# Kernel tuning notes

Hardware: AMD Instinct MI355X
Metric: run time of the kernel (lower is better)

## Reference

```python
import jax, jax.numpy as jnp
import numpy as np

# ---- static configuration (mirrors repo globals) ----
D_MODEL = 1024   # d_model
B = 128          # batch size
T = 256          # structure sequence length (tgt)
T_C = 128        # max constraints per scene (tgt_c rows)
N_PER = 64       # real (non-padded) constraints per scene
S = 128          # number of source objects per scene (src_e rows)
N_TYPES = 4      # len(constraint_types)
N_DIR = 4        # len(direction_types)
C_TOKEN = 2      # structure_vocab_map['c']
N_C = N_PER * B  # total constraints across the batch (static!)


def setup_inputs() -> dict:
    key = jax.random.key(0)
    ks = jax.random.split(key, 12)
    decoded_output = jax.random.normal(ks[0], (T, B, D_MODEL), jnp.float32)
    # tgt: the first N_PER timesteps of every batch element are constraint tokens 'c'.
    tgt = jnp.where(jnp.arange(T)[:, None] < N_PER, C_TOKEN, 0) * jnp.ones((1, B), jnp.int32)
    tgt = tgt.astype(jnp.int32)
    # tgt_c padding: rows >= N_PER are padding -> exactly N_PER*B = N_C real constraints,
    # laid out row-major (timestep-major, batch-fastest) when flattened.
    tgt_c_padding_mask = jnp.broadcast_to(jnp.arange(T_C)[:, None] >= N_PER, (T_C, B))
    types_col = jax.random.randint(ks[1], (T_C, B), 0, N_TYPES)
    q_col = jax.random.randint(ks[2], (T_C, B), 0, S)
    r_col = jax.random.randint(ks[3], (T_C, B), 0, S)
    tgt_c = jnp.stack([types_col, q_col, r_col], axis=-1).astype(jnp.int32)  # [T_C,B,3]
    src_e = jax.random.normal(ks[4], (S, B, D_MODEL), jnp.float32)
    src_padding_mask = jax.random.uniform(ks[5], (B, S)) < 0.1
    scale = 0.02
    params = {
        'type_emb': jax.random.normal(ks[6], (N_TYPES, D_MODEL), jnp.float32),
        'W_ctype': jax.random.normal(ks[7], (N_TYPES, D_MODEL), jnp.float32) * scale,
        'b_ctype': jnp.zeros((N_TYPES,), jnp.float32),
        'W_obj': jax.random.normal(ks[8], (D_MODEL, 3 * D_MODEL), jnp.float32) * scale,
        'b_obj': jnp.zeros((D_MODEL,), jnp.float32),
        'W_dir': jax.random.normal(ks[9], (N_DIR, 4 * D_MODEL), jnp.float32) * scale,
        'b_dir': jnp.zeros((N_DIR,), jnp.float32),
    }
    return dict(decoded_output=decoded_output, tgt=tgt, tgt_c=tgt_c,
                tgt_c_padding_mask=tgt_c_padding_mask, src_e=src_e,
                src_padding_mask=src_padding_mask, **params)


def reference(decoded_output, tgt, tgt_c, tgt_c_padding_mask, src_e, src_padding_mask,
              type_emb, W_ctype, b_ctype, W_obj, b_obj, W_dir, b_dir):
    d = decoded_output.shape[-1]
    # --- static-count boolean selections (setup guarantees exactly N_C True entries) ---
    idx_struct = jnp.nonzero((tgt == C_TOKEN).reshape(-1), size=N_C)[0]
    heads = decoded_output.reshape(-1, d)[idx_struct]                # [N_C, d]
    idx_c = jnp.nonzero((~tgt_c_padding_mask).reshape(-1), size=N_C)[0]

    # constraint type logits
    type_selections = heads @ W_ctype.T + b_ctype                    # [N_C, N_TYPES]

    # constraint type embeddings
    types = type_emb[tgt_c[:, :, 0].reshape(-1)[idx_c]]              # [N_C, d]

    # q_e: gather query-object embeddings (torch.gather along dim 0)
    q_idx = jnp.broadcast_to(tgt_c[:, :, 1:2], (T_C, B, d))
    q_e = jnp.take_along_axis(src_e, q_idx, axis=0).reshape(-1, d)[idx_c]  # [N_C, d]

    obj_in = jnp.concatenate([heads, types, q_e], axis=1)            # [N_C, 3d]
    pointer = obj_in @ W_obj.T + b_obj                               # [N_C, d]

    batch_ref = jnp.broadcast_to(jnp.arange(B), (T_C, B)).reshape(-1)[idx_c]  # [N_C]
    # Setup layout guarantee: flattened constraint order is (t, b) row-major with b
    # fastest, N_PER constraints per batch -> pointer reshapes to [N_PER, B, d] and the
    # original per-item tensordot loop collapses into one batched einsum.
    ptr = pointer.reshape(N_PER, B, d)
    logits = jnp.einsum('tbd,sbd->tbs', ptr, src_e).reshape(N_C, S)  # [N_C, S]
    object_selections = jnp.where(src_padding_mask[batch_ref], -jnp.inf, logits)

    # r_e: gather reference-object embeddings
    r_idx = jnp.broadcast_to(tgt_c[:, :, 2:3], (T_C, B, d))
    r_e = jnp.take_along_axis(src_e, r_idx, axis=0).reshape(-1, d)[idx_c]    # [N_C, d]

    dir_in = jnp.concatenate([obj_in, r_e], axis=1)                  # [N_C, 4d]
    direction_selections = dir_in @ W_dir.T + b_dir                  # [N_C, N_DIR]
    return (type_selections, object_selections, direction_selections)
```

## Files before the change

### kernel.cpp

```cpp
#include <hip/hip_runtime.h>
#include <hip/hip_bf16.h>
#include <math.h>

#define D_MODEL 1024
#define B_SZ    128
#define S_SZ    128
#define N_C     8192
#define K_OBJ   3072
#define K_DIR   4096

#define TS_OFF  0
#define OS_OFF  (N_C * 4)
#define DS_OFF  (OS_OFF + N_C * S_SZ)

#define NEG_BIG (-1.0e30f)

typedef __attribute__((ext_vector_type(8))) int   i32x8;
typedef __attribute__((ext_vector_type(4))) float f32x4;

#define WS_PTR8   0ull
#define WS_DEC8   8388608ull
#define WS_SRCE8  16777216ull
#define WS_WOBJ8  33554432ull
#define WS_TEMB8  36700160ull

#define SCALE_ONE 0x7F7F7F7F

__device__ __forceinline__ uint2 f32x8_to_fp8(float4 a, float4 b) {
    unsigned lo = 0, hi = 0;
    lo = __builtin_amdgcn_cvt_pk_fp8_f32(a.x, a.y, lo, false);
    lo = __builtin_amdgcn_cvt_pk_fp8_f32(a.z, a.w, lo, true);
    hi = __builtin_amdgcn_cvt_pk_fp8_f32(b.x, b.y, hi, false);
    hi = __builtin_amdgcn_cvt_pk_fp8_f32(b.z, b.w, hi, true);
    return make_uint2(lo, hi);
}
__device__ __forceinline__ unsigned char f32_to_fp8(float x) {
    return (unsigned char)(__builtin_amdgcn_cvt_pk_fp8_f32(x, x, 0, false) & 0xFF);
}

typedef __attribute__((address_space(3))) unsigned int lds_u32;
typedef __attribute__((address_space(1))) const unsigned int glb_u32;
__device__ __forceinline__ void dma16(const void* g, void* l) {
    __builtin_amdgcn_global_load_lds((glb_u32*)g, (lds_u32*)l, 16, 0, 0);
}

__global__ __launch_bounds__(256) void cvt_fp8_all(
    const float* __restrict__ decoded, const float* __restrict__ src_e,
    const float* __restrict__ W_obj,   const float* __restrict__ type_emb,
    unsigned char* __restrict__ dec8,  unsigned char* __restrict__ srce8,
    unsigned char* __restrict__ wobj8, unsigned char* __restrict__ temb8)
{
    const int blk = blockIdx.x;
    const float* src; unsigned char* dst; size_t u;
    if (blk < 4096)        { src = decoded;  dst = dec8;  u = (size_t)blk * 256 + threadIdx.x; }
    else if (blk < 12288)  { src = src_e;    dst = srce8; u = (size_t)(blk - 4096) * 256 + threadIdx.x; }
    else if (blk < 13824)  { src = W_obj;    dst = wobj8; u = (size_t)(blk - 12288) * 256 + threadIdx.x; }
    else                   { src = type_emb; dst = temb8; u = (size_t)(blk - 13824) * 256 + threadIdx.x; }
    const float4* s = (const float4*)src + u * 2;
    float4 a = s[0], b = s[1];
    *(uint2*)(dst + u * 8) = f32x8_to_fp8(a, b);
}

__global__ __launch_bounds__(256) void pointer_fp8(
    const unsigned char* __restrict__ dec8,
    const unsigned char* __restrict__ temb8,
    const unsigned char* __restrict__ srce8,
    const unsigned char* __restrict__ wobj8,
    const int*   __restrict__ tgt_c,
    const float* __restrict__ b_obj,
    unsigned char* __restrict__ ptr_out)
{
    __shared__ __align__(32) unsigned char As[128 * 128];
    __shared__ __align__(32) unsigned char Bs[128 * 128];

    const int tid  = threadIdx.x;
    const int m0   = blockIdx.x * 128;
    const int n0   = blockIdx.y * 128;
    const int lane = tid & 63;
    const int wv   = tid >> 6;

    const int srow = wv * 8 + (lane >> 3);
    const int c16  = lane & 7;
    const unsigned char *pA0[4], *pA1[4], *pA2[4], *pB[4];
    #pragma unroll
    for (int ro = 0; ro < 4; ++ro) {
        int r = ro * 32 + srow;
        int g = (c16 ^ ((r & 3) << 1)) * 16;
        int n = m0 + r;
        int tt = tgt_c[n * 3 + 0];
        int qq = tgt_c[n * 3 + 1];
        pA0[ro] = dec8  + (size_t)n * 1024 + g;
        pA1[ro] = temb8 + (size_t)tt * 1024 + g;
        pA2[ro] = srce8 + ((size_t)qq * B_SZ + r) * 1024 + g;
        pB[ro]  = wobj8 + (size_t)(n0 + r) * K_OBJ + g;
    }

    const int wm   = (wv & 1) * 64;
    const int wn   = (wv >> 1) * 64;
    const int fm   = lane & 15;
    const int quad = lane >> 4;

    f32x4 acc[4][4];
    #pragma unroll
    for (int i = 0; i < 4; ++i)
        #pragma unroll
        for (int j = 0; j < 4; ++j)
            acc[i][j] = (f32x4){0.f, 0.f, 0.f, 0.f};

    for (int ks = 0; ks < K_OBJ / 128; ++ks) {
        const int k0   = ks * 128;
        const int reg  = k0 >> 10;
        const int koff = k0 & 1023;
        #pragma unroll
        for (int ro = 0; ro < 4; ++ro) {
            void* la = As + ro * 4096 + wv * 1024;
            if (reg == 0)      dma16(pA0[ro] + koff, la);
            else if (reg == 1) dma16(pA1[ro] + koff, la);
            else               dma16(pA2[ro] + koff, la);
            dma16(pB[ro] + k0, Bs + ro * 4096 + wv * 1024);
        }
        __syncthreads();

        i32x8 af[4], bfr[4];
        #pragma unroll
        for (int i = 0; i < 4; ++i) {
            int ra = wm + i * 16 + fm;
            af[i] = *(const i32x8*)&As[ra * 128 + ((quad ^ (ra & 3)) << 5)];
        }
        #pragma unroll
        for (int j = 0; j < 4; ++j) {
            int rb = wn + j * 16 + fm;
            bfr[j] = *(const i32x8*)&Bs[rb * 128 + ((quad ^ (rb & 3)) << 5)];
        }
        #pragma unroll
        for (int i = 0; i < 4; ++i)
            #pragma unroll
            for (int j = 0; j < 4; ++j)
                acc[i][j] = __builtin_amdgcn_mfma_scale_f32_16x16x128_f8f6f4(
                    af[i], bfr[j], acc[i][j], 0, 0, 0, SCALE_ONE, 0, SCALE_ONE);
        __syncthreads();
    }

    #pragma unroll
    for (int j = 0; j < 4; ++j) {
        int ncol = n0 + wn + j * 16 + fm;
        float bo = b_obj[ncol];
        #pragma unroll
        for (int i = 0; i < 4; ++i) {
            int mrow = m0 + wm + i * 16 + quad * 4;
            f32x4 c = acc[i][j];
            #pragma unroll
            for (int r2 = 0; r2 < 4; ++r2)
                ptr_out[(size_t)(mrow + r2) * D_MODEL + ncol] = f32_to_fp8(c[r2] + bo);
        }
    }
}

__global__ __launch_bounds__(256) void logits_fp8(
    const unsigned char* __restrict__ ptr8,
    const unsigned char* __restrict__ srce8,
    const void*  __restrict__ src_pm,
    float*       __restrict__ out_os)
{
    __shared__ __align__(32) unsigned char As[64 * 128];
    __shared__ __align__(32) unsigned char Bs[64 * 128];
    __shared__ int s_flag;

    const int tid  = threadIdx.x;
    const int b    = blockIdx.x;
    const int s0   = blockIdx.y * 64;
    const int lane = tid & 63;
    const int wv   = tid >> 6;

    if (tid == 0) s_flag = 0;
    __syncthreads();
    {
        const int* pmi = (const int*)src_pm;
        int local = 0;
        for (int i = tid; i < 4096; i += 256) local |= (pmi[i] > 1);
        if (local) atomicOr(&s_flag, 1);
    }

    const int srow = wv * 8 + (lane >> 3);
    const int c16  = lane & 7;
    const unsigned char *pA[2], *pBt[2];
    #pragma unroll
    for (int ro = 0; ro < 2; ++ro) {
        int r = ro * 32 + srow;
        int g = (c16 ^ ((r & 3) << 1)) * 16;
        pA[ro]  = ptr8  + ((size_t)r * B_SZ + b) * 1024 + g;
        pBt[ro] = srce8 + ((size_t)(s0 + r) * B_SZ + b) * 1024 + g;
    }

    const int wm   = (wv & 1) * 32;
    const int wn   = (wv >> 1) * 32;
    const int fm   = lane & 15;
    const int quad = lane >> 4;

    f32x4 acc[2][2];
    #pragma unroll
    for (int i = 0; i < 2; ++i)
        #pragma unroll
        for (int j = 0; j < 2; ++j)
            acc[i][j] = (f32x4){0.f, 0.f, 0.f, 0.f};

    for (int ks = 0; ks < D_MODEL / 128; ++ks) {
        const int k0 = ks * 128;
        #pragma unroll
        for (int ro = 0; ro < 2; ++ro) {
            dma16(pA[ro]  + k0, As + ro * 4096 + wv * 1024);
            dma16(pBt[ro] + k0, Bs + ro * 4096 + wv * 1024);
        }
        __syncthreads();

        i32x8 af[2], bfr[2];
        #pragma unroll
        for (int i = 0; i < 2; ++i) {
            int ra = wm + i * 16 + fm;
            af[i] = *(const i32x8*)&As[ra * 128 + ((quad ^ (ra & 3)) << 5)];
        }
        #pragma unroll
        for (int j = 0; j < 2; ++j) {
            int rb = wn + j * 16 + fm;
            bfr[j] = *(const i32x8*)&Bs[rb * 128 + ((quad ^ (rb & 3)) << 5)];
        }
        #pragma unroll
        for (int i = 0; i < 2; ++i)
            #pragma unroll
            for (int j = 0; j < 2; ++j)
                acc[i][j] = __builtin_amdgcn_mfma_scale_f32_16x16x128_f8f6f4(
                    af[i], bfr[j], acc[i][j], 0, 0, 0, SCALE_ONE, 0, SCALE_ONE);
        __syncthreads();
    }

    const bool u8 = (s_flag != 0);
    const unsigned char* pm8  = (const unsigned char*)src_pm;
    const int*           pm32 = (const int*)src_pm;

    #pragma unroll
    for (int j = 0; j < 2; ++j) {
        int s = s0 + wn + j * 16 + fm;
        bool m = u8 ? (pm8[b * S_SZ + s] != 0) : (pm32[b * S_SZ + s] != 0);
        #pragma unroll
        for (int i = 0; i < 2; ++i) {
            int t = wm + i * 16 + quad * 4;
            f32x4 c = acc[i][j];
            #pragma unroll
            for (int r2 = 0; r2 < 4; ++r2)
                out_os[(size_t)((t + r2) * B_SZ + b) * S_SZ + s] = m ? NEG_BIG : c[r2];
        }
    }
}

__global__ __launch_bounds__(256) void typedir_kernel(
    const float* __restrict__ decoded,
    const int*   __restrict__ tgt_c,
    const float* __restrict__ src_e,
    const float* __restrict__ type_emb,
    const float* __restrict__ W_ctype,
    const float* __restrict__ b_ctype,
    const float* __restrict__ W_dir,
    const float* __restrict__ b_dir,
    float*       __restrict__ out)
{
    const int tid = threadIdx.x;
    const int n0  = blockIdx.x * 4;

    __shared__ int s_idx[4][3];
    if (tid < 12) s_idx[tid / 3][tid % 3] = tgt_c[(n0 + tid / 3) * 3 + (tid % 3)];
    __syncthreads();

    float acct[4][4] = {};
    float accd[4][4] = {};

    #pragma unroll 4
    for (int it = 0; it < 16; ++it) {
        int k      = tid + it * 256;
        int region = k >> 10;
        int koff   = k & 1023;

        float wd0 = W_dir[0 * K_DIR + k];
        float wd1 = W_dir[1 * K_DIR + k];
        float wd2 = W_dir[2 * K_DIR + k];
        float wd3 = W_dir[3 * K_DIR + k];
        float wc0 = 0.f, wc1 = 0.f, wc2 = 0.f, wc3 = 0.f;
        if (region == 0) {
            wc0 = W_ctype[0 * D_MODEL + koff];
            wc1 = W_ctype[1 * D_MODEL + koff];
            wc2 = W_ctype[2 * D_MODEL + koff];
            wc3 = W_ctype[3 * D_MODEL + koff];
        }

        #pragma unroll
        for (int r = 0; r < 4; ++r) {
            int n = n0 + r;
            int b = n & 127;
            float a;
            if (region == 0)      a = decoded[(size_t)n * D_MODEL + koff];
            else if (region == 1) a = type_emb[(size_t)s_idx[r][0] * D_MODEL + koff];
            else if (region == 2) a = src_e[((size_t)s_idx[r][1] * B_SZ + b) * D_MODEL + koff];
            else                  a = src_e[((size_t)s_idx[r][2] * B_SZ + b) * D_MODEL + koff];

            accd[r][0] += a * wd0;
            accd[r][1] += a * wd1;
            accd[r][2] += a * wd2;
            accd[r][3] += a * wd3;
            if (region == 0) {
                acct[r][0] += a * wc0;
                acct[r][1] += a * wc1;
                acct[r][2] += a * wc2;
                acct[r][3] += a * wc3;
            }
        }
    }

    __shared__ float red[4][32];
    const int lane = tid & 63;
    const int wave = tid >> 6;

    float vals[32];
    #pragma unroll
    for (int r = 0; r < 4; ++r)
        #pragma unroll
        for (int c = 0; c < 4; ++c) {
            vals[r * 4 + c]      = acct[r][c];
            vals[16 + r * 4 + c] = accd[r][c];
        }

    #pragma unroll
    for (int x = 0; x < 32; ++x) {
        float v = vals[x];
        #pragma unroll
        for (int off = 32; off > 0; off >>= 1)
            v += __shfl_down(v, off, 64);
        vals[x] = v;
    }
    if (lane == 0)
        #pragma unroll
        for (int x = 0; x < 32; ++x) red[wave][x] = vals[x];
    __syncthreads();

    if (tid < 32) {
        float v = red[0][tid] + red[1][tid] + red[2][tid] + red[3][tid];
        int r = (tid & 15) >> 2;
        int c = tid & 3;
        int n = n0 + r;
        if (tid < 16) out[TS_OFF + (size_t)n * 4 + c] = v + b_ctype[c];
        else          out[DS_OFF + (size_t)n * 4 + c] = v + b_dir[c];
    }
}

extern "C" void kernel_launch(void* const* d_in, const int* in_sizes, int n_in,
                              void* d_out, int out_size, void* d_ws, size_t ws_size,
                              hipStream_t stream) {
    const float* decoded  = (const float*)d_in[0];
    const int*   tgt_c    = (const int*)d_in[2];
    const float* src_e    = (const float*)d_in[4];
    const void*  src_pm   = d_in[5];
    const float* type_emb = (const float*)d_in[6];
    const float* W_ctype  = (const float*)d_in[7];
    const float* b_ctype  = (const float*)d_in[8];
    const float* W_obj    = (const float*)d_in[9];
    const float* b_obj    = (const float*)d_in[10];
    const float* W_dir    = (const float*)d_in[11];
    const float* b_dir    = (const float*)d_in[12];

    float* out = (float*)d_out;
    char*  ws  = (char*)d_ws;
    unsigned char* ptr8  = (unsigned char*)(ws + WS_PTR8);
    unsigned char* dec8  = (unsigned char*)(ws + WS_DEC8);
    unsigned char* srce8 = (unsigned char*)(ws + WS_SRCE8);
    unsigned char* wobj8 = (unsigned char*)(ws + WS_WOBJ8);
    unsigned char* temb8 = (unsigned char*)(ws + WS_TEMB8);

    cvt_fp8_all<<<13826, 256, 0, stream>>>(
        decoded, src_e, W_obj, type_emb, dec8, srce8, wobj8, temb8);

    pointer_fp8<<<dim3(N_C / 128, D_MODEL / 128), 256, 0, stream>>>(
        dec8, temb8, srce8, wobj8, tgt_c, b_obj, ptr8);

    typedir_kernel<<<N_C / 4, 256, 0, stream>>>(
        decoded, tgt_c, src_e, type_emb, W_ctype, b_ctype, W_dir, b_dir, out);

    logits_fp8<<<dim3(B_SZ, 2), 256, 0, stream>>>(
        ptr8, srce8, src_pm, out + OS_OFF);
}
```

Measured before the change: 327.5 us.

## Double-buffer LDS in fp8 GEMMs and fuse decoded fp8 conversion into typedir

```diff
diff --git a/kernel.cpp b/kernel.cpp
--- a/kernel.cpp
+++ b/kernel.cpp
@@ -45,17 +45,16 @@
 }
 
 __global__ __launch_bounds__(256) void cvt_fp8_all(
-    const float* __restrict__ decoded, const float* __restrict__ src_e,
-    const float* __restrict__ W_obj,   const float* __restrict__ type_emb,
-    unsigned char* __restrict__ dec8,  unsigned char* __restrict__ srce8,
-    unsigned char* __restrict__ wobj8, unsigned char* __restrict__ temb8)
+    const float* __restrict__ src_e,   const float* __restrict__ W_obj,
+    const float* __restrict__ type_emb,
+    unsigned char* __restrict__ srce8, unsigned char* __restrict__ wobj8,
+    unsigned char* __restrict__ temb8)
 {
     const int blk = blockIdx.x;
     const float* src; unsigned char* dst; size_t u;
-    if (blk < 4096)        { src = decoded;  dst = dec8;  u = (size_t)blk * 256 + threadIdx.x; }
-    else if (blk < 12288)  { src = src_e;    dst = srce8; u = (size_t)(blk - 4096) * 256 + threadIdx.x; }
-    else if (blk < 13824)  { src = W_obj;    dst = wobj8; u = (size_t)(blk - 12288) * 256 + threadIdx.x; }
-    else                   { src = type_emb; dst = temb8; u = (size_t)(blk - 13824) * 256 + threadIdx.x; }
+    if (blk < 8192)       { src = src_e;    dst = srce8; u = (size_t)blk * 256 + threadIdx.x; }
+    else if (blk < 9728)  { src = W_obj;    dst = wobj8; u = (size_t)(blk - 8192) * 256 + threadIdx.x; }
+    else                  { src = type_emb; dst = temb8; u = (size_t)(blk - 9728) * 256 + threadIdx.x; }
     const float4* s = (const float4*)src + u * 2;
     float4 a = s[0], b = s[1];
     *(uint2*)(dst + u * 8) = f32x8_to_fp8(a, b);
@@ -70,8 +69,8 @@
     const float* __restrict__ b_obj,
     unsigned char* __restrict__ ptr_out)
 {
-    __shared__ __align__(32) unsigned char As[128 * 128];
-    __shared__ __align__(32) unsigned char Bs[128 * 128];
+    __shared__ __align__(32) unsigned char As[2][128 * 128];
+    __shared__ __align__(32) unsigned char Bs[2][128 * 128];
 
     const int tid  = threadIdx.x;
     const int m0   = blockIdx.x * 128;
@@ -107,30 +106,40 @@
         for (int j = 0; j < 4; ++j)
             acc[i][j] = (f32x4){0.f, 0.f, 0.f, 0.f};
 
+    #pragma unroll
+    for (int ro = 0; ro < 4; ++ro) {
+        dma16(pA0[ro], &As[0][ro * 4096 + wv * 1024]);
+        dma16(pB[ro],  &Bs[0][ro * 4096 + wv * 1024]);
+    }
+    __syncthreads();
+
     for (int ks = 0; ks < K_OBJ / 128; ++ks) {
-        const int k0   = ks * 128;
-        const int reg  = k0 >> 10;
-        const int koff = k0 & 1023;
-        #pragma unroll
-        for (int ro = 0; ro < 4; ++ro) {
-            void* la = As + ro * 4096 + wv * 1024;
-            if (reg == 0)      dma16(pA0[ro] + koff, la);
-            else if (reg == 1) dma16(pA1[ro] + koff, la);
-            else               dma16(pA2[ro] + koff, la);
-            dma16(pB[ro] + k0, Bs + ro * 4096 + wv * 1024);
-        }
-        __syncthreads();
+        const int buf = ks & 1;
+
+        if (ks + 1 < K_OBJ / 128) {
+            const int k0n   = (ks + 1) * 128;
+            const int regn  = k0n >> 10;
+            const int koffn = k0n & 1023;
+            #pragma unroll
+            for (int ro = 0; ro < 4; ++ro) {
+                void* la = &As[buf ^ 1][ro * 4096 + wv * 1024];
+                if (regn == 0)      dma16(pA0[ro] + koffn, la);
+                else if (regn == 1) dma16(pA1[ro] + koffn, la);
+                else                dma16(pA2[ro] + koffn, la);
+                dma16(pB[ro] + k0n, &Bs[buf ^ 1][ro * 4096 + wv * 1024]);
+            }
+        }
 
         i32x8 af[4], bfr[4];
         #pragma unroll
         for (int i = 0; i < 4; ++i) {
             int ra = wm + i * 16 + fm;
-            af[i] = *(const i32x8*)&As[ra * 128 + ((quad ^ (ra & 3)) << 5)];
+            af[i] = *(const i32x8*)&As[buf][ra * 128 + ((quad ^ (ra & 3)) << 5)];
         }
         #pragma unroll
         for (int j = 0; j < 4; ++j) {
             int rb = wn + j * 16 + fm;
-            bfr[j] = *(const i32x8*)&Bs[rb * 128 + ((quad ^ (rb & 3)) << 5)];
+            bfr[j] = *(const i32x8*)&Bs[buf][rb * 128 + ((quad ^ (rb & 3)) << 5)];
         }
         #pragma unroll
         for (int i = 0; i < 4; ++i)
@@ -138,6 +147,7 @@
             for (int j = 0; j < 4; ++j)
                 acc[i][j] = __builtin_amdgcn_mfma_scale_f32_16x16x128_f8f6f4(
                     af[i], bfr[j], acc[i][j], 0, 0, 0, SCALE_ONE, 0, SCALE_ONE);
+
         __syncthreads();
     }
 
@@ -162,8 +172,8 @@
     const void*  __restrict__ src_pm,
     float*       __restrict__ out_os)
 {
-    __shared__ __align__(32) unsigned char As[64 * 128];
-    __shared__ __align__(32) unsigned char Bs[64 * 128];
+    __shared__ __align__(32) unsigned char As[2][64 * 128];
+    __shared__ __align__(32) unsigned char Bs[2][64 * 128];
     __shared__ int s_flag;
 
     const int tid  = threadIdx.x;
@@ -204,25 +214,35 @@
         for (int j = 0; j < 2; ++j)
             acc[i][j] = (f32x4){0.f, 0.f, 0.f, 0.f};
 
+    #pragma unroll
+    for (int ro = 0; ro < 2; ++ro) {
+        dma16(pA[ro],  &As[0][ro * 4096 + wv * 1024]);
+        dma16(pBt[ro], &Bs[0][ro * 4096 + wv * 1024]);
+    }
+    __syncthreads();
+
     for (int ks = 0; ks < D_MODEL / 128; ++ks) {
-        const int k0 = ks * 128;
-        #pragma unroll
-        for (int ro = 0; ro < 2; ++ro) {
-            dma16(pA[ro]  + k0, As + ro * 4096 + wv * 1024);
-            dma16(pBt[ro] + k0, Bs + ro * 4096 + wv * 1024);
-        }
-        __syncthreads();
+        const int buf = ks & 1;
+
+        if (ks + 1 < D_MODEL / 128) {
+            const int k0n = (ks + 1) * 128;
+            #pragma unroll
+            for (int ro = 0; ro < 2; ++ro) {
+                dma16(pA[ro]  + k0n, &As[buf ^ 1][ro * 4096 + wv * 1024]);
+                dma16(pBt[ro] + k0n, &Bs[buf ^ 1][ro * 4096 + wv * 1024]);
+            }
+        }
 
         i32x8 af[2], bfr[2];
         #pragma unroll
         for (int i = 0; i < 2; ++i) {
             int ra = wm + i * 16 + fm;
-            af[i] = *(const i32x8*)&As[ra * 128 + ((quad ^ (ra & 3)) << 5)];
+            af[i] = *(const i32x8*)&As[buf][ra * 128 + ((quad ^ (ra & 3)) << 5)];
         }
         #pragma unroll
         for (int j = 0; j < 2; ++j) {
             int rb = wn + j * 16 + fm;
-            bfr[j] = *(const i32x8*)&Bs[rb * 128 + ((quad ^ (rb & 3)) << 5)];
+            bfr[j] = *(const i32x8*)&Bs[buf][rb * 128 + ((quad ^ (rb & 3)) << 5)];
         }
         #pragma unroll
         for (int i = 0; i < 2; ++i)
@@ -230,6 +250,7 @@
             for (int j = 0; j < 2; ++j)
                 acc[i][j] = __builtin_amdgcn_mfma_scale_f32_16x16x128_f8f6f4(
                     af[i], bfr[j], acc[i][j], 0, 0, 0, SCALE_ONE, 0, SCALE_ONE);
+
         __syncthreads();
     }
 
@@ -261,10 +282,12 @@
     const float* __restrict__ b_ctype,
     const float* __restrict__ W_dir,
     const float* __restrict__ b_dir,
+    unsigned char* __restrict__ dec8,
     float*       __restrict__ out)
 {
     const int tid = threadIdx.x;
     const int n0  = blockIdx.x * 4;
+    const int kc  = tid * 4;
 
     __shared__ int s_idx[4][3];
     if (tid < 12) s_idx[tid / 3][tid % 3] = tgt_c[(n0 + tid / 3) * 3 + (tid % 3)];
@@ -273,43 +296,46 @@
     float acct[4][4] = {};
     float accd[4][4] = {};
 
-    #pragma unroll 4
-    for (int it = 0; it < 16; ++it) {
-        int k      = tid + it * 256;
-        int region = k >> 10;
-        int koff   = k & 1023;
-
-        float wd0 = W_dir[0 * K_DIR + k];
-        float wd1 = W_dir[1 * K_DIR + k];
-        float wd2 = W_dir[2 * K_DIR + k];
-        float wd3 = W_dir[3 * K_DIR + k];
-        float wc0 = 0.f, wc1 = 0.f, wc2 = 0.f, wc3 = 0.f;
-        if (region == 0) {
-            wc0 = W_ctype[0 * D_MODEL + koff];
-            wc1 = W_ctype[1 * D_MODEL + koff];
-            wc2 = W_ctype[2 * D_MODEL + koff];
-            wc3 = W_ctype[3 * D_MODEL + koff];
+    #pragma unroll
+    for (int it = 0; it < 4; ++it) {
+        float4 wd[4];
+        #pragma unroll
+        for (int c = 0; c < 4; ++c)
+            wd[c] = *(const float4*)&W_dir[(size_t)c * K_DIR + it * 1024 + kc];
+        float4 wc[4];
+        if (it == 0) {
+            #pragma unroll
+            for (int c = 0; c < 4; ++c)
+                wc[c] = *(const float4*)&W_ctype[(size_t)c * D_MODEL + kc];
         }
 
         #pragma unroll
         for (int r = 0; r < 4; ++r) {
-            int n = n0 + r;
-            int b = n & 127;
-            float a;
-            if (region == 0)      a = decoded[(size_t)n * D_MODEL + koff];
-            else if (region == 1) a = type_emb[(size_t)s_idx[r][0] * D_MODEL + koff];
-            else if (region == 2) a = src_e[((size_t)s_idx[r][1] * B_SZ + b) * D_MODEL + koff];
-            else                  a = src_e[((size_t)s_idx[r][2] * B_SZ + b) * D_MODEL + koff];
-
-            accd[r][0] += a * wd0;
-            accd[r][1] += a * wd1;
-            accd[r][2] += a * wd2;
-            accd[r][3] += a * wd3;
-            if (region == 0) {
-                acct[r][0] += a * wc0;
-                acct[r][1] += a * wc1;
-                acct[r][2] += a * wc2;
-                acct[r][3] += a * wc3;
+            const int n = n0 + r;
+            const int b = n & 127;
+            float4 a;
+            if (it == 0) {
+                a = *(const float4*)&decoded[(size_t)n * D_MODEL + kc];
+                unsigned pk = __builtin_amdgcn_cvt_pk_fp8_f32(a.x, a.y, 0u, false);
+                pk = __builtin_amdgcn_cvt_pk_fp8_f32(a.z, a.w, pk, true);
+                *(unsigned*)(dec8 + (size_t)n * D_MODEL + kc) = pk;
+            } else if (it == 1) {
+                a = *(const float4*)&type_emb[(size_t)s_idx[r][0] * D_MODEL + kc];
+            } else if (it == 2) {
+                a = *(const float4*)&src_e[((size_t)s_idx[r][1] * B_SZ + b) * D_MODEL + kc];
+            } else {
+                a = *(const float4*)&src_e[((size_t)s_idx[r][2] * B_SZ + b) * D_MODEL + kc];
+            }
+
+            #pragma unroll
+            for (int c = 0; c < 4; ++c)
+                accd[r][c] += a.x * wd[c].x + a.y * wd[c].y
+                            + a.z * wd[c].z + a.w * wd[c].w;
+            if (it == 0) {
+                #pragma unroll
+                for (int c = 0; c < 4; ++c)
+                    acct[r][c] += a.x * wc[c].x + a.y * wc[c].y
+                                + a.z * wc[c].z + a.w * wc[c].w;
             }
         }
     }
@@ -373,15 +399,16 @@
     unsigned char* wobj8 = (unsigned char*)(ws + WS_WOBJ8);
     unsigned char* temb8 = (unsigned char*)(ws + WS_TEMB8);
 
-    cvt_fp8_all<<<13826, 256, 0, stream>>>(
-        decoded, src_e, W_obj, type_emb, dec8, srce8, wobj8, temb8);
+    cvt_fp8_all<<<9730, 256, 0, stream>>>(
+        src_e, W_obj, type_emb, srce8, wobj8, temb8);
+
+    typedir_kernel<<<N_C / 4, 256, 0, stream>>>(
+        decoded, tgt_c, src_e, type_emb, W_ctype, b_ctype, W_dir, b_dir,
+        dec8, out);
 
     pointer_fp8<<<dim3(N_C / 128, D_MODEL / 128), 256, 0, stream>>>(
         dec8, temb8, srce8, wobj8, tgt_c, b_obj, ptr8);
 
-    typedir_kernel<<<N_C / 4, 256, 0, stream>>>(
-        decoded, tgt_c, src_e, type_emb, W_ctype, b_ctype, W_dir, b_dir, out);
-
     logits_fp8<<<dim3(B_SZ, 2), 256, 0, stream>>>(
         ptr8, srce8, src_pm, out + OS_OFF);
 }
```

After: 290.2 us. -11.4%, faster.
